# Kernel tuning notes

Hardware: AMD Instinct MI355X
Metric: run time of the kernel (lower is better)

## Reference

```python
import jax, jax.numpy as jnp
import numpy as np

N_ROLES = 6
EPS = 1e-5

def _ln(x, scale, bias):
    m = jnp.mean(x, axis=-1, keepdims=True)
    v = jnp.var(x, axis=-1, keepdims=True)
    return (x - m) * jax.lax.rsqrt(v + EPS) * scale + bias

def setup_inputs() -> dict:
    key = jax.random.key(0)
    ks = jax.random.split(key, 20)
    T, B, D_OBS, H, A = 32, 1024, 256, 512, 32
    inp = {
        'rnn_states': jax.random.normal(ks[0], (B, H), jnp.float32),
        'obs': jax.random.normal(ks[1], (T, B, D_OBS), jnp.float32),
        'resets': jnp.zeros((T, B), jnp.float32),
        'available_actions': jnp.ones((T, B, A), jnp.float32),
        'role_ids': jax.random.randint(ks[2], (T, B), 0, N_ROLES, jnp.int32),
        # feature norm over obs_dim
        'fn_scale': jnp.ones((D_OBS,), jnp.float32),
        'fn_bias': jnp.zeros((D_OBS,), jnp.float32),
        # base MLP: obs_dim->512->512, each followed by LayerNorm
        'W0': jax.random.normal(ks[3], (D_OBS, H), jnp.float32) * 0.02,
        'b0': jnp.zeros((H,), jnp.float32),
        'ln0_scale': jnp.ones((H,), jnp.float32),
        'ln0_bias': jnp.zeros((H,), jnp.float32),
        'W1': jax.random.normal(ks[4], (H, H), jnp.float32) * 0.02,
        'b1': jnp.zeros((H,), jnp.float32),
        'ln1_scale': jnp.ones((H,), jnp.float32),
        'ln1_bias': jnp.zeros((H,), jnp.float32),
        # per-role routes: obs_dim->128->H (stacked over roles)
        'Wr0': jax.random.normal(ks[5], (N_ROLES, D_OBS, 128), jnp.float32) * 0.02,
        'br0': jnp.zeros((N_ROLES, 128), jnp.float32),
        'Wr1': jax.random.normal(ks[6], (N_ROLES, 128, H), jnp.float32) * 0.02,
        'br1': jnp.zeros((N_ROLES, H), jnp.float32),
        # per-role heads: H->64->32->action_dim (stacked over roles)
        'Wh0': jax.random.normal(ks[7], (N_ROLES, H, 64), jnp.float32) * 0.02,
        'bh0': jnp.zeros((N_ROLES, 64), jnp.float32),
        'Wh1': jax.random.normal(ks[8], (N_ROLES, 64, 32), jnp.float32) * 0.02,
        'bh1': jnp.zeros((N_ROLES, 32), jnp.float32),
        'Wh2': jax.random.normal(ks[9], (N_ROLES, 32, A), jnp.float32) * 0.02,
        'bh2': jnp.zeros((N_ROLES, A), jnp.float32),
    }
    return inp

def _gather_by_role(all_values, role_ids):
    # all_values: (K, T, B, F); role_ids: (T, B) -> (T, B, F)
    idx = role_ids[None, :, :, None].astype(jnp.int32)
    return jnp.take_along_axis(all_values, idx, axis=0)[0]

def reference(rnn_states, obs, resets, available_actions, role_ids,
              fn_scale, fn_bias, W0, b0, ln0_scale, ln0_bias,
              W1, b1, ln1_scale, ln1_bias,
              Wr0, br0, Wr1, br1,
              Wh0, bh0, Wh1, bh1, Wh2, bh2):
    # feature normalization on raw obs
    obs_n = _ln(obs, fn_scale, fn_bias)
    # shared base MLP (relu + LayerNorm after each Dense)
    e = _ln(jax.nn.relu(obs_n @ W0 + b0), ln0_scale, ln0_bias)
    e = _ln(jax.nn.relu(e @ W1 + b1), ln1_scale, ln1_bias)
    # per-role pre-GRU residual routes on (normalized) obs
    r = jax.nn.relu(jnp.einsum('tbi,kih->ktbh', obs_n, Wr0) + br0[:, None, None, :])
    r = jax.nn.relu(jnp.einsum('ktbh,kho->ktbo', r, Wr1) + br1[:, None, None, :])
    e = e + _gather_by_role(r, role_ids)
    # no recurrent policy configured: rnn_states pass through
    # per-role heads -> all logits (K, T, B, A)
    h = jax.nn.relu(jnp.einsum('tbh,khf->ktbf', e, Wh0) + bh0[:, None, None, :])
    h = jax.nn.relu(jnp.einsum('ktbf,kfg->ktbg', h, Wh1) + bh1[:, None, None, :])
    all_logits = jnp.einsum('ktbg,kga->ktba', h, Wh2) + bh2[:, None, None, :]
    logits = _gather_by_role(all_logits, role_ids)
    logits = jnp.where(available_actions > 0.5, logits, jnp.full_like(logits, -1e10))
    return rnn_states, logits
```

## Files before the change

kernel.cpp:

```cpp
#include <hip/hip_runtime.h>
#include <stdint.h>

typedef unsigned short u16;
typedef unsigned int u32;

using bf16x8 = __attribute__((ext_vector_type(8))) short;
using f32x4  = __attribute__((ext_vector_type(4))) float;

#define DEVINL __device__ __forceinline__

DEVINL float b2f(u16 u) { return __builtin_bit_cast(float, (u32)u << 16); }
DEVINL u16 f2b(float f) {
  u32 u = __builtin_bit_cast(u32, f);
  u += 0x7FFFu + ((u >> 16) & 1u);
  return (u16)(u >> 16);
}

DEVINL void gll16(const u16* src, u16* dst) {
  __builtin_amdgcn_global_load_lds(
      (const __attribute__((address_space(1))) void*)(uintptr_t)src,
      (__attribute__((address_space(3))) void*)(uintptr_t)dst, 16, 0, 0);
}

#define MFMA __builtin_amdgcn_mfma_f32_16x16x32_bf16
#define NROLE 6
#define PROWS 33152
#define PBLK  518

__global__ __launch_bounds__(256) void role_count(
    const int* __restrict__ rid, int* __restrict__ blkCnt)
{
  __shared__ int h[NROLE];
  if (threadIdx.x < NROLE) h[threadIdx.x] = 0;
  __syncthreads();
  atomicAdd(&h[rid[blockIdx.x * 256 + threadIdx.x]], 1);
  __syncthreads();
  if (threadIdx.x < NROLE) blkCnt[blockIdx.x * NROLE + threadIdx.x] = h[threadIdx.x];
}

__global__ __launch_bounds__(256) void fill2(
    const int* __restrict__ rid, const int* __restrict__ blkCnt,
    int* __restrict__ bucket, int* __restrict__ pbaseOut, int* __restrict__ cntArr)
{
  __shared__ int c[128 * NROLE];
  __shared__ int preArr[NROLE], scnt[NROLE], pb[NROLE + 1], h[NROLE];
  const int tid = threadIdx.x;
  const int bx = blockIdx.x;
  for (int i = tid; i < 128 * NROLE; i += 256) c[i] = blkCnt[i];
  if (tid < NROLE) h[tid] = 0;
  __syncthreads();
  if (tid < NROLE) {
    int k = tid, run = 0, pre = 0;
    for (int b = 0; b < 128; ++b) { if (b == bx) pre = run; run += c[b * NROLE + k]; }
    scnt[k] = run; preArr[k] = pre;
  }
  __syncthreads();
  if (tid == 0) {
    pb[0] = 0;
    for (int k = 0; k < NROLE; ++k) pb[k + 1] = pb[k] + ((scnt[k] + 63) & ~63);
  }
  __syncthreads();
  if (bx == 0) {
    if (tid <= NROLE) pbaseOut[tid] = pb[tid];
    if (tid < NROLE) cntArr[tid] = scnt[tid];
    for (int k = 0; k < NROLE; ++k)
      for (int p = pb[k] + scnt[k] + tid; p < pb[k + 1]; p += 256) bucket[p] = 0;
    for (int p = pb[NROLE] + tid; p < PROWS; p += 256) bucket[p] = 0;
  }
  int i = bx * 256 + tid;
  int k = rid[i];
  int pos = atomicAdd(&h[k], 1);
  bucket[pb[k] + preArr[k] + pos] = i;
}

DEVINL void tp_tile(const float* __restrict__ s, u16* __restrict__ d,
                    int R, int C, int bx, int by, int z)
{
  __shared__ u16 tile[32][33];
  const size_t mstride = (size_t)R * C;
  s += (size_t)z * mstride;
  d += (size_t)z * mstride;
  int r0 = bx * 32, c0 = by * 32;
  int tx = threadIdx.x & 31, ty = threadIdx.x >> 5;
#pragma unroll
  for (int i = 0; i < 32; i += 8)
    tile[ty + i][tx] = f2b(s[(size_t)(r0 + ty + i) * C + (c0 + tx)]);
  __syncthreads();
#pragma unroll
  for (int i = 0; i < 32; i += 8)
    d[(size_t)(c0 + ty + i) * R + (r0 + tx)] = tile[tx][ty + i];
}

__global__ __launch_bounds__(256) void mega0(
    const float* W0, const float* W1, const float* Wr0, const float* Wr1, const float* Wh0,
    u16* W0t, u16* W1t, u16* Wr0t, u16* Wr1t, u16* Wh0t,
    const float* __restrict__ obs, const float* __restrict__ fn_s,
    const float* __restrict__ fn_b, u16* __restrict__ obs_nB,
    const int* __restrict__ bucket,
    const float* __restrict__ rnn, float* __restrict__ outRnn)
{
  int b = blockIdx.x;
  const int tid = threadIdx.x;
  if (b < 1152) {
    if (b < 128)      {            tp_tile(W0, W0t, 256, 512, b % 8,  b / 8, 0); }
    else if (b < 384) { b -= 128;  tp_tile(W1, W1t, 512, 512, b % 16, b / 16, 0); }
    else if (b < 576) { b -= 384;  int t = b / 8;  tp_tile(Wr0, Wr0t, 256, 128, b % 8,  t % 4,  t / 4); }
    else if (b < 960) { b -= 576;  int t = b / 4;  tp_tile(Wr1, Wr1t, 128, 512, b % 4,  t % 16, t / 16); }
    else              { b -= 960;  int t = b / 16; tp_tile(Wh0, Wh0t, 512, 64,  b % 16, t % 2,  t / 2); }
  } else if (b < 1152 + PROWS / 16) {
    b -= 1152;
    const int lane = tid & 63, wave = tid >> 6;
#pragma unroll
    for (int it = 0; it < 4; ++it) {
      int p = b * 16 + wave * 4 + it;
      int g = bucket[p];
      const float* xr = obs + (size_t)g * 256 + lane * 4;
      float x[4] __attribute__((aligned(16)));
      *(float4*)x = *(const float4*)xr;
      float s = 0.f, s2 = 0.f;
#pragma unroll
      for (int q = 0; q < 4; ++q) { s += x[q]; s2 += x[q] * x[q]; }
#pragma unroll
      for (int o = 32; o > 0; o >>= 1) { s += __shfl_xor(s, o, 64); s2 += __shfl_xor(s2, o, 64); }
      float m = s * (1.f / 256.f);
      float v = s2 * (1.f / 256.f) - m * m;
      float inv = rsqrtf(v + 1e-5f);
      u16 yu[4] __attribute__((aligned(8)));
#pragma unroll
      for (int q = 0; q < 4; ++q)
        yu[q] = f2b((x[q] - m) * inv * fn_s[lane * 4 + q] + fn_b[lane * 4 + q]);
      *(uint2*)(obs_nB + (size_t)p * 256 + lane * 4) = *(uint2*)yu;
    }
  } else {
    b -= 1152 + PROWS / 16;
    const float4* src = (const float4*)rnn;
    float4* dst = (float4*)outRnn;
    int base = (b * 256 + tid) * 4;
#pragma unroll
    for (int i = 0; i < 4; ++i) dst[base + i] = src[base + i];
  }
}

template <int K>
DEVINL void gemm_ln_body(
    const u16* __restrict__ A, const u16* __restrict__ Bt,
    const float* __restrict__ bias, const float* __restrict__ lnsc,
    const float* __restrict__ lnbi, u16* __restrict__ C, int bx)
{
  constexpr int BK = 64, NI = K / BK;
  __shared__ __align__(16) u16 As[2][64 * BK];
  __shared__ float redS[64][4];
  __shared__ float redSS[64][4];
  __shared__ float prm[1536];
  const int tid = threadIdx.x;
  const int rowBase = bx * 64;
  const int lane = tid & 63, wave = tid >> 6;
#pragma unroll
  for (int i = tid; i < 512; i += 256) {
    prm[i] = bias[i]; prm[512 + i] = lnsc[i]; prm[1024 + i] = lnbi[i];
  }
  u32 aOff[2];
#pragma unroll
  for (int r = 0; r < 2; ++r) {
    int row = r * 32 + (tid >> 3);
    aOff[r] = (u32)(rowBase + row) * (u32)K + (u32)(((tid & 7) ^ (row & 7)) * 8);
  }
  const int quad = lane >> 4, lm = lane & 15, l7 = lm & 7;
  const int wn = wave * 128;
  u32 bOff[8];
#pragma unroll
  for (int j = 0; j < 8; ++j)
    bOff[j] = (u32)(wn + j * 16 + lm) * (u32)K + (u32)(quad * 8);

  f32x4 acc[4][8] = {};

#pragma unroll
  for (int r = 0; r < 2; ++r)
    gll16(A + aOff[r], &As[0][r * 2048 + wave * 512]);
  bf16x8 bP[8];
#pragma unroll
  for (int j = 0; j < 8; ++j)
    bP[j] = *(const bf16x8*)(Bt + bOff[j]);
  __syncthreads();

  for (int i = 0; i < NI; ++i) {
    const u16* Ab = As[i & 1];
    if (i + 1 < NI) {
#pragma unroll
      for (int r = 0; r < 2; ++r)
        gll16(A + aOff[r] + (i + 1) * BK, &As[(i + 1) & 1][r * 2048 + wave * 512]);
    }
    bf16x8 bN[8];
#pragma unroll
    for (int j = 0; j < 8; ++j)
      bN[j] = *(const bf16x8*)(Bt + bOff[j] + i * BK + 32);
    bf16x8 af[4];
#pragma unroll
    for (int i2 = 0; i2 < 4; ++i2)
      af[i2] = *(const bf16x8*)&Ab[(i2 * 16 + lm) * 64 + ((quad ^ l7) * 8)];
#pragma unroll
    for (int i2 = 0; i2 < 4; ++i2)
#pragma unroll
      for (int j = 0; j < 8; ++j)
        acc[i2][j] = MFMA(af[i2], bP[j], acc[i2][j], 0, 0, 0);
    if (i + 1 < NI) {
#pragma unroll
      for (int j = 0; j < 8; ++j)
        bP[j] = *(const bf16x8*)(Bt + bOff[j] + (i + 1) * BK);
    }
#pragma unroll
    for (int i2 = 0; i2 < 4; ++i2)
      af[i2] = *(const bf16x8*)&Ab[(i2 * 16 + lm) * 64 + (((quad + 4) ^ l7) * 8)];
#pragma unroll
    for (int i2 = 0; i2 < 4; ++i2)
#pragma unroll
      for (int j = 0; j < 8; ++j)
        acc[i2][j] = MFMA(af[i2], bN[j], acc[i2][j], 0, 0, 0);
    __syncthreads();
  }

#pragma unroll
  for (int i2 = 0; i2 < 4; ++i2) {
#pragma unroll
    for (int r2 = 0; r2 < 4; ++r2) {
      float s = 0.f, ss = 0.f;
#pragma unroll
      for (int j = 0; j < 8; ++j) {
        float v = fmaxf(acc[i2][j][r2] + prm[wn + j * 16 + lm], 0.f);
        acc[i2][j][r2] = v;
        s += v; ss += v * v;
      }
#pragma unroll
      for (int o = 1; o < 16; o <<= 1) { s += __shfl_xor(s, o, 64); ss += __shfl_xor(ss, o, 64); }
      if (lm == 0) {
        int rowL = i2 * 16 + quad * 4 + r2;
        redS[rowL][wave] = s;
        redSS[rowL][wave] = ss;
      }
    }
  }
  __syncthreads();
#pragma unroll
  for (int i2 = 0; i2 < 4; ++i2) {
#pragma unroll
    for (int r2 = 0; r2 < 4; ++r2) {
      int rowL = i2 * 16 + quad * 4 + r2;
      float ts  = redS[rowL][0] + redS[rowL][1] + redS[rowL][2] + redS[rowL][3];
      float tss = redSS[rowL][0] + redSS[rowL][1] + redSS[rowL][2] + redSS[rowL][3];
      float m = ts * (1.f / 512.f);
      float var = tss * (1.f / 512.f) - m * m;
      float inv = rsqrtf(var + 1e-5f);
      size_t base = (size_t)(rowBase + rowL) * 512;
#pragma unroll
      for (int j = 0; j < 8; ++j) {
        int col = wn + j * 16 + lm;
        float y = (acc[i2][j][r2] - m) * inv * prm[512 + col] + prm[1024 + col];
        C[base + col] = f2b(y);
      }
    }
  }
}

DEVINL void route0_body(
    const u16* __restrict__ A, const u16* __restrict__ Wr0t,
    const float* __restrict__ br0, u16* __restrict__ r1out,
    const int* __restrict__ pbase, int bx)
{
  constexpr int K = 256, NI = 4;
  __shared__ __align__(16) u16 As0[2][64 * 64];
  const int tid = threadIdx.x;
  const int rowBase = bx * 64;
  if (rowBase >= pbase[NROLE]) return;
  int role = 0;
  while (rowBase >= pbase[role + 1]) ++role;
  const int lane = tid & 63, wave = tid >> 6;
  const int quad = lane >> 4, lm = lane & 15, l7 = lm & 7;
  u32 aOff[2];
#pragma unroll
  for (int r = 0; r < 2; ++r) {
    int row = r * 32 + (tid >> 3);
    aOff[r] = (u32)(rowBase + row) * (u32)K + (u32)(((tid & 7) ^ (row & 7)) * 8);
  }
  const int wn0 = wave * 32;
  const u16* B0 = Wr0t + (size_t)role * 128 * 256;
  u32 bOff[2];
#pragma unroll
  for (int j = 0; j < 2; ++j)
    bOff[j] = (u32)(wn0 + j * 16 + lm) * (u32)K + (u32)(quad * 8);

  f32x4 acc[4][2] = {};
#pragma unroll
  for (int r = 0; r < 2; ++r)
    gll16(A + aOff[r], &As0[0][r * 2048 + wave * 512]);
  bf16x8 bP[2];
#pragma unroll
  for (int j = 0; j < 2; ++j) bP[j] = *(const bf16x8*)(B0 + bOff[j]);
  __syncthreads();

  for (int i = 0; i < NI; ++i) {
    const u16* Ab = As0[i & 1];
    if (i + 1 < NI) {
#pragma unroll
      for (int r = 0; r < 2; ++r)
        gll16(A + aOff[r] + (i + 1) * 64, &As0[(i + 1) & 1][r * 2048 + wave * 512]);
    }
    bf16x8 bN[2];
#pragma unroll
    for (int j = 0; j < 2; ++j) bN[j] = *(const bf16x8*)(B0 + bOff[j] + i * 64 + 32);
    bf16x8 af[4];
#pragma unroll
    for (int i2 = 0; i2 < 4; ++i2)
      af[i2] = *(const bf16x8*)&Ab[(i2 * 16 + lm) * 64 + ((quad ^ l7) * 8)];
#pragma unroll
    for (int i2 = 0; i2 < 4; ++i2)
#pragma unroll
      for (int j = 0; j < 2; ++j)
        acc[i2][j] = MFMA(af[i2], bP[j], acc[i2][j], 0, 0, 0);
    if (i + 1 < NI) {
#pragma unroll
      for (int j = 0; j < 2; ++j) bP[j] = *(const bf16x8*)(B0 + bOff[j] + (i + 1) * 64);
    }
#pragma unroll
    for (int i2 = 0; i2 < 4; ++i2)
      af[i2] = *(const bf16x8*)&Ab[(i2 * 16 + lm) * 64 + (((quad + 4) ^ l7) * 8)];
#pragma unroll
    for (int i2 = 0; i2 < 4; ++i2)
#pragma unroll
      for (int j = 0; j < 2; ++j)
        acc[i2][j] = MFMA(af[i2], bN[j], acc[i2][j], 0, 0, 0);
    __syncthreads();
  }
  float bia[2];
#pragma unroll
  for (int j = 0; j < 2; ++j) bia[j] = br0[role * 128 + wn0 + j * 16 + lm];
#pragma unroll
  for (int i2 = 0; i2 < 4; ++i2) {
#pragma unroll
    for (int r2 = 0; r2 < 4; ++r2) {
      int row = rowBase + i2 * 16 + quad * 4 + r2;
#pragma unroll
      for (int j = 0; j < 2; ++j) {
        int col = wn0 + j * 16 + lm;
        r1out[(size_t)row * 128 + col] = f2b(fmaxf(acc[i2][j][r2] + bia[j], 0.f));
      }
    }
  }
}

__global__ __launch_bounds__(256, 2) void g256_r0(
    const u16* __restrict__ obs_nB, const u16* __restrict__ W0t,
    const float* __restrict__ b0, const float* __restrict__ ln0s,
    const float* __restrict__ ln0b, u16* __restrict__ bufA,
    const u16* __restrict__ Wr0t, const float* __restrict__ br0,
    u16* __restrict__ r1out, const int* __restrict__ pbase)
{
  if (blockIdx.x < PBLK)
    gemm_ln_body<256>(obs_nB, W0t, b0, ln0s, ln0b, bufA, blockIdx.x);
  else
    route0_body(obs_nB, Wr0t, br0, r1out, pbase, blockIdx.x - PBLK);
}

__global__ __launch_bounds__(256, 2) void gemm512(
    const u16* __restrict__ bufA, const u16* __restrict__ W1t,
    const float* __restrict__ b1, const float* __restrict__ ln1s,
    const float* __restrict__ ln1b, u16* __restrict__ bufB)
{
  gemm_ln_body<512>(bufA, W1t, b1, ln1s, ln1b, bufB, blockIdx.x);
}

__global__ __launch_bounds__(256, 2) void route1_k(
    const u16* __restrict__ r1, const u16* __restrict__ Wr1t,
    const float* __restrict__ br1, const u16* __restrict__ e,
    u16* __restrict__ ea, const int* __restrict__ pbase)
{
  constexpr int K = 128, NI = 2;
  __shared__ __align__(16) u16 As[2][64 * 64];
  const int tid = threadIdx.x;
  const int rowBase = blockIdx.x * 64;
  if (rowBase >= pbase[NROLE]) return;
  int role = 0;
  while (rowBase >= pbase[role + 1]) ++role;
  const int lane = tid & 63, wave = tid >> 6;
  const int quad = lane >> 4, lm = lane & 15, l7 = lm & 7;
  u32 aOff[2];
#pragma unroll
  for (int r = 0; r < 2; ++r) {
    int row = r * 32 + (tid >> 3);
    aOff[r] = (u32)(rowBase + row) * (u32)K + (u32)(((tid & 7) ^ (row & 7)) * 8);
  }
  const int wn = wave * 128;
  const u16* B1 = Wr1t + (size_t)role * 512 * 128;
  u32 bOff[8];
#pragma unroll
  for (int j = 0; j < 8; ++j)
    bOff[j] = (u32)(wn + j * 16 + lm) * (u32)K + (u32)(quad * 8);

  f32x4 acc[4][8] = {};
#pragma unroll
  for (int r = 0; r < 2; ++r)
    gll16(r1 + aOff[r], &As[0][r * 2048 + wave * 512]);
  bf16x8 bP[8];
#pragma unroll
  for (int j = 0; j < 8; ++j) bP[j] = *(const bf16x8*)(B1 + bOff[j]);
  __syncthreads();

  for (int i = 0; i < NI; ++i) {
    const u16* Ab = As[i & 1];
    if (i + 1 < NI) {
#pragma unroll
      for (int r = 0; r < 2; ++r)
        gll16(r1 + aOff[r] + (i + 1) * 64, &As[(i + 1) & 1][r * 2048 + wave * 512]);
    }
    bf16x8 bN[8];
#pragma unroll
    for (int j = 0; j < 8; ++j) bN[j] = *(const bf16x8*)(B1 + bOff[j] + i * 64 + 32);
    bf16x8 af[4];
#pragma unroll
    for (int i2 = 0; i2 < 4; ++i2)
      af[i2] = *(const bf16x8*)&Ab[(i2 * 16 + lm) * 64 + ((quad ^ l7) * 8)];
#pragma unroll
    for (int i2 = 0; i2 < 4; ++i2)
#pragma unroll
      for (int j = 0; j < 8; ++j)
        acc[i2][j] = MFMA(af[i2], bP[j], acc[i2][j], 0, 0, 0);
    if (i + 1 < NI) {
#pragma unroll
      for (int j = 0; j < 8; ++j) bP[j] = *(const bf16x8*)(B1 + bOff[j] + (i + 1) * 64);
    }
#pragma unroll
    for (int i2 = 0; i2 < 4; ++i2)
      af[i2] = *(const bf16x8*)&Ab[(i2 * 16 + lm) * 64 + (((quad + 4) ^ l7) * 8)];
#pragma unroll
    for (int i2 = 0; i2 < 4; ++i2)
#pragma unroll
      for (int j = 0; j < 8; ++j)
        acc[i2][j] = MFMA(af[i2], bN[j], acc[i2][j], 0, 0, 0);
    __syncthreads();
  }
  float bia[8];
#pragma unroll
  for (int j = 0; j < 8; ++j) bia[j] = br1[role * 512 + wn + j * 16 + lm];
#pragma unroll
  for (int i2 = 0; i2 < 4; ++i2) {
#pragma unroll
    for (int r2 = 0; r2 < 4; ++r2) {
      size_t row = (size_t)(rowBase + i2 * 16 + quad * 4 + r2);
#pragma unroll
      for (int j = 0; j < 8; ++j) {
        int col = wn + j * 16 + lm;
        float v = fmaxf(acc[i2][j][r2] + bia[j], 0.f) + b2f(e[row * 512 + col]);
        ea[row * 512 + col] = f2b(v);
      }
    }
  }
}

__global__ __launch_bounds__(256, 2) void head_all(
    const u16* __restrict__ ea, const u16* __restrict__ Wh0t,
    const float* __restrict__ bh0,
    const float* __restrict__ Wh1, const float* __restrict__ bh1,
    const float* __restrict__ Wh2, const float* __restrict__ bh2,
    const float* __restrict__ avail, const int* __restrict__ bucket,
    const int* __restrict__ pbase, const int* __restrict__ cntArr,
    float* __restrict__ outLogits)
{
  constexpr int K = 512, NI = 8;
  __shared__ __align__(16) u16 As[2][64 * 64];
  __shared__ u16 h0s[64 * 68];
  __shared__ float h1s[64 * 36];
  const int tid = threadIdx.x;
  const int rowBase = blockIdx.x * 64;
  if (rowBase >= pbase[NROLE]) return;
  int role = 0;
  while (rowBase >= pbase[role + 1]) ++role;
  const int lane = tid & 63, wave = tid >> 6;
  const int quad = lane >> 4, lm = lane & 15, l7 = lm & 7;
  u32 aOff[2];
#pragma unroll
  for (int r = 0; r < 2; ++r) {
    int row = r * 32 + (tid >> 3);
    aOff[r] = (u32)(rowBase + row) * (u32)K + (u32)(((tid & 7) ^ (row & 7)) * 8);
  }
  const int col0 = wave * 16 + lm;
  const u16* B2 = Wh0t + (size_t)role * 64 * 512;
  const u32 bOff = (u32)col0 * (u32)K + (u32)(quad * 8);

  f32x4 acc[4] = {};
#pragma unroll
  for (int r = 0; r < 2; ++r)
    gll16(ea + aOff[r], &As[0][r * 2048 + wave * 512]);
  bf16x8 bP = *(const bf16x8*)(B2 + bOff);
  __syncthreads();

  for (int i = 0; i < NI; ++i) {
    const u16* Ab = As[i & 1];
    if (i + 1 < NI) {
#pragma unroll
      for (int r = 0; r < 2; ++r)
        gll16(ea + aOff[r] + (i + 1) * 64, &As[(i + 1) & 1][r * 2048 + wave * 512]);
    }
    bf16x8 bN = *(const bf16x8*)(B2 + bOff + i * 64 + 32);
    bf16x8 af[4];
#pragma unroll
    for (int i2 = 0; i2 < 4; ++i2)
      af[i2] = *(const bf16x8*)&Ab[(i2 * 16 + lm) * 64 + ((quad ^ l7) * 8)];
#pragma unroll
    for (int i2 = 0; i2 < 4; ++i2)
      acc[i2] = MFMA(af[i2], bP, acc[i2], 0, 0, 0);
    if (i + 1 < NI) bP = *(const bf16x8*)(B2 + bOff + (i + 1) * 64);
#pragma unroll
    for (int i2 = 0; i2 < 4; ++i2)
      af[i2] = *(const bf16x8*)&Ab[(i2 * 16 + lm) * 64 + (((quad + 4) ^ l7) * 8)];
#pragma unroll
    for (int i2 = 0; i2 < 4; ++i2)
      acc[i2] = MFMA(af[i2], bN, acc[i2], 0, 0, 0);
    __syncthreads();
  }
  {
    float b2v = bh0[role * 64 + col0];
#pragma unroll
    for (int i2 = 0; i2 < 4; ++i2)
#pragma unroll
      for (int r2 = 0; r2 < 4; ++r2) {
        int row = i2 * 16 + quad * 4 + r2;
        h0s[row * 68 + col0] = f2b(fmaxf(acc[i2][r2] + b2v, 0.f));
      }
  }
  __syncthreads();

  {
    const int r = tid >> 2;
    const int n0 = (tid & 3) * 8;
    const float* W1k = Wh1 + (size_t)role * 64 * 32;
    const float* W2k = Wh2 + (size_t)role * 32 * 32;
    float4 a1a = *(const float4*)(bh1 + role * 32 + n0);
    float4 a1b = *(const float4*)(bh1 + role * 32 + n0 + 4);
#pragma unroll 8
    for (int j = 0; j < 64; ++j) {
      float hj = b2f(h0s[r * 68 + j]);
      float4 wa = *(const float4*)(W1k + j * 32 + n0);
      float4 wb = *(const float4*)(W1k + j * 32 + n0 + 4);
      a1a.x += hj * wa.x; a1a.y += hj * wa.y; a1a.z += hj * wa.z; a1a.w += hj * wa.w;
      a1b.x += hj * wb.x; a1b.y += hj * wb.y; a1b.z += hj * wb.z; a1b.w += hj * wb.w;
    }
    h1s[r * 36 + n0 + 0] = fmaxf(a1a.x, 0.f);
    h1s[r * 36 + n0 + 1] = fmaxf(a1a.y, 0.f);
    h1s[r * 36 + n0 + 2] = fmaxf(a1a.z, 0.f);
    h1s[r * 36 + n0 + 3] = fmaxf(a1a.w, 0.f);
    h1s[r * 36 + n0 + 4] = fmaxf(a1b.x, 0.f);
    h1s[r * 36 + n0 + 5] = fmaxf(a1b.y, 0.f);
    h1s[r * 36 + n0 + 6] = fmaxf(a1b.z, 0.f);
    h1s[r * 36 + n0 + 7] = fmaxf(a1b.w, 0.f);
    __syncthreads();
    float4 a2a = *(const float4*)(bh2 + role * 32 + n0);
    float4 a2b = *(const float4*)(bh2 + role * 32 + n0 + 4);
#pragma unroll 8
    for (int n = 0; n < 32; ++n) {
      float hn = h1s[r * 36 + n];
      float4 wa = *(const float4*)(W2k + n * 32 + n0);
      float4 wb = *(const float4*)(W2k + n * 32 + n0 + 4);
      a2a.x += hn * wa.x; a2a.y += hn * wa.y; a2a.z += hn * wa.z; a2a.w += hn * wa.w;
      a2b.x += hn * wb.x; a2b.y += hn * wb.y; a2b.z += hn * wb.z; a2b.w += hn * wb.w;
    }
    int local = rowBase + r - pbase[role];
    if (local < cntArr[role]) {
      int g = bucket[rowBase + r];
      float4 ava = *(const float4*)(avail + (size_t)g * 32 + n0);
      float4 avb = *(const float4*)(avail + (size_t)g * 32 + n0 + 4);
      float4 oa, ob;
      oa.x = (ava.x > 0.5f) ? a2a.x : -1e10f;
      oa.y = (ava.y > 0.5f) ? a2a.y : -1e10f;
      oa.z = (ava.z > 0.5f) ? a2a.z : -1e10f;
      oa.w = (ava.w > 0.5f) ? a2a.w : -1e10f;
      ob.x = (avb.x > 0.5f) ? a2b.x : -1e10f;
      ob.y = (avb.y > 0.5f) ? a2b.y : -1e10f;
      ob.z = (avb.z > 0.5f) ? a2b.z : -1e10f;
      ob.w = (avb.w > 0.5f) ? a2b.w : -1e10f;
      *(float4*)(outLogits + (size_t)g * 32 + n0) = oa;
      *(float4*)(outLogits + (size_t)g * 32 + n0 + 4) = ob;
    }
  }
}

extern "C" void kernel_launch(void* const* d_in, const int* in_sizes, int n_in,
                              void* d_out, int out_size, void* d_ws, size_t ws_size,
                              hipStream_t stream)
{
  const float* rnn  = (const float*)d_in[0];
  const float* obs  = (const float*)d_in[1];
  const float* avail= (const float*)d_in[3];
  const int*   rid  = (const int*)d_in[4];
  const float* fn_s = (const float*)d_in[5];
  const float* fn_b = (const float*)d_in[6];
  const float* W0   = (const float*)d_in[7];
  const float* b0   = (const float*)d_in[8];
  const float* ln0s = (const float*)d_in[9];
  const float* ln0b = (const float*)d_in[10];
  const float* W1   = (const float*)d_in[11];
  const float* b1   = (const float*)d_in[12];
  const float* ln1s = (const float*)d_in[13];
  const float* ln1b = (const float*)d_in[14];
  const float* Wr0  = (const float*)d_in[15];
  const float* br0  = (const float*)d_in[16];
  const float* Wr1  = (const float*)d_in[17];
  const float* br1  = (const float*)d_in[18];
  const float* Wh0  = (const float*)d_in[19];
  const float* bh0  = (const float*)d_in[20];
  const float* Wh1  = (const float*)d_in[21];
  const float* bh1  = (const float*)d_in[22];
  const float* Wh2  = (const float*)d_in[23];
  const float* bh2  = (const float*)d_in[24];

  char* w = (char*)d_ws;
  auto carve = [&](size_t bytes) { char* p = w; w += (bytes + 255) & ~(size_t)255; return p; };
  u16* obs_nB = (u16*)carve((size_t)PROWS * 256 * 2);
  u16* bufA   = (u16*)carve((size_t)PROWS * 512 * 2);
  u16* bufB   = (u16*)carve((size_t)PROWS * 512 * 2);
  u16* r1buf  = (u16*)carve((size_t)PROWS * 128 * 2);
  u16* W0t    = (u16*)carve((size_t)512 * 256 * 2);
  u16* W1t    = (u16*)carve((size_t)512 * 512 * 2);
  u16* Wr0t   = (u16*)carve((size_t)6 * 128 * 256 * 2);
  u16* Wr1t   = (u16*)carve((size_t)6 * 512 * 128 * 2);
  u16* Wh0t   = (u16*)carve((size_t)6 * 64 * 512 * 2);
  int* bucket = (int*)carve((size_t)PROWS * 4);
  int* blkCnt = (int*)carve((size_t)128 * NROLE * 4);
  int* pbase  = (int*)carve(256);
  int* cntArr = (int*)carve(256);

  float* outLogits = (float*)d_out + (size_t)1024 * 512;

  role_count<<<128, 256, 0, stream>>>(rid, blkCnt);
  fill2<<<128, 256, 0, stream>>>(rid, blkCnt, bucket, pbase, cntArr);

  mega0<<<1152 + PROWS / 16 + 128, 256, 0, stream>>>(
      W0, W1, Wr0, Wr1, Wh0, W0t, W1t, Wr0t, Wr1t, Wh0t,
      obs, fn_s, fn_b, obs_nB, bucket, rnn, (float*)d_out);

  g256_r0<<<2 * PBLK, 256, 0, stream>>>(obs_nB, W0t, b0, ln0s, ln0b, bufA,
                                        Wr0t, br0, r1buf, pbase);

  gemm512<<<PBLK, 256, 0, stream>>>(bufA, W1t, b1, ln1s, ln1b, bufB);

  route1_k<<<PBLK, 256, 0, stream>>>(r1buf, Wr1t, br1, bufB, bufA, pbase);

  head_all<<<PBLK, 256, 0, stream>>>(bufA, Wh0t, bh0, Wh1, bh1, Wh2, bh2,
                                     avail, bucket, pbase, cntArr, outLogits);
}
```

Measured before the change: 301.3 us.

## Fuse pipeline into two row-block kernels keeping activations in LDS

Result: slower. 368.6 us (+22.4%).

```diff
diff --git a/kernel.cpp b/kernel.cpp
--- a/kernel.cpp
+++ b/kernel.cpp
@@ -38,14 +38,14 @@
   if (threadIdx.x < NROLE) blkCnt[blockIdx.x * NROLE + threadIdx.x] = h[threadIdx.x];
 }
 
-__global__ __launch_bounds__(256) void fill2(
+DEVINL void fill_body(
     const int* __restrict__ rid, const int* __restrict__ blkCnt,
-    int* __restrict__ bucket, int* __restrict__ pbaseOut, int* __restrict__ cntArr)
+    int* __restrict__ bucket, int* __restrict__ pbaseOut, int* __restrict__ cntArr,
+    int bx)
 {
   __shared__ int c[128 * NROLE];
   __shared__ int preArr[NROLE], scnt[NROLE], pb[NROLE + 1], h[NROLE];
   const int tid = threadIdx.x;
-  const int bx = blockIdx.x;
   for (int i = tid; i < 128 * NROLE; i += 256) c[i] = blkCnt[i];
   if (tid < NROLE) h[tid] = 0;
   __syncthreads();
@@ -91,13 +91,12 @@
     d[(size_t)(c0 + ty + i) * R + (r0 + tx)] = tile[tx][ty + i];
 }
 
-__global__ __launch_bounds__(256) void mega0(
+__global__ __launch_bounds__(256) void prep(
     const float* W0, const float* W1, const float* Wr0, const float* Wr1, const float* Wh0,
     u16* W0t, u16* W1t, u16* Wr0t, u16* Wr1t, u16* Wh0t,
-    const float* __restrict__ obs, const float* __restrict__ fn_s,
-    const float* __restrict__ fn_b, u16* __restrict__ obs_nB,
-    const int* __restrict__ bucket,
-    const float* __restrict__ rnn, float* __restrict__ outRnn)
+    const float* __restrict__ rnn, float* __restrict__ outRnn,
+    const int* __restrict__ rid, const int* __restrict__ blkCnt,
+    int* __restrict__ bucket, int* __restrict__ pbase, int* __restrict__ cntArr)
 {
   int b = blockIdx.x;
   const int tid = threadIdx.x;
@@ -107,274 +106,30 @@
     else if (b < 576) { b -= 384;  int t = b / 8;  tp_tile(Wr0, Wr0t, 256, 128, b % 8,  t % 4,  t / 4); }
     else if (b < 960) { b -= 576;  int t = b / 4;  tp_tile(Wr1, Wr1t, 128, 512, b % 4,  t % 16, t / 16); }
     else              { b -= 960;  int t = b / 16; tp_tile(Wh0, Wh0t, 512, 64,  b % 16, t % 2,  t / 2); }
-  } else if (b < 1152 + PROWS / 16) {
+  } else if (b < 1280) {
     b -= 1152;
-    const int lane = tid & 63, wave = tid >> 6;
-#pragma unroll
-    for (int it = 0; it < 4; ++it) {
-      int p = b * 16 + wave * 4 + it;
-      int g = bucket[p];
-      const float* xr = obs + (size_t)g * 256 + lane * 4;
-      float x[4] __attribute__((aligned(16)));
-      *(float4*)x = *(const float4*)xr;
-      float s = 0.f, s2 = 0.f;
-#pragma unroll
-      for (int q = 0; q < 4; ++q) { s += x[q]; s2 += x[q] * x[q]; }
-#pragma unroll
-      for (int o = 32; o > 0; o >>= 1) { s += __shfl_xor(s, o, 64); s2 += __shfl_xor(s2, o, 64); }
-      float m = s * (1.f / 256.f);
-      float v = s2 * (1.f / 256.f) - m * m;
-      float inv = rsqrtf(v + 1e-5f);
-      u16 yu[4] __attribute__((aligned(8)));
-#pragma unroll
-      for (int q = 0; q < 4; ++q)
-        yu[q] = f2b((x[q] - m) * inv * fn_s[lane * 4 + q] + fn_b[lane * 4 + q]);
-      *(uint2*)(obs_nB + (size_t)p * 256 + lane * 4) = *(uint2*)yu;
-    }
-  } else {
-    b -= 1152 + PROWS / 16;
     const float4* src = (const float4*)rnn;
     float4* dst = (float4*)outRnn;
     int base = (b * 256 + tid) * 4;
 #pragma unroll
     for (int i = 0; i < 4; ++i) dst[base + i] = src[base + i];
-  }
-}
-
-template <int K>
-DEVINL void gemm_ln_body(
-    const u16* __restrict__ A, const u16* __restrict__ Bt,
-    const float* __restrict__ bias, const float* __restrict__ lnsc,
-    const float* __restrict__ lnbi, u16* __restrict__ C, int bx)
-{
-  constexpr int BK = 64, NI = K / BK;
-  __shared__ __align__(16) u16 As[2][64 * BK];
-  __shared__ float redS[64][4];
-  __shared__ float redSS[64][4];
-  __shared__ float prm[1536];
-  const int tid = threadIdx.x;
-  const int rowBase = bx * 64;
-  const int lane = tid & 63, wave = tid >> 6;
-#pragma unroll
-  for (int i = tid; i < 512; i += 256) {
-    prm[i] = bias[i]; prm[512 + i] = lnsc[i]; prm[1024 + i] = lnbi[i];
-  }
-  u32 aOff[2];
-#pragma unroll
-  for (int r = 0; r < 2; ++r) {
-    int row = r * 32 + (tid >> 3);
-    aOff[r] = (u32)(rowBase + row) * (u32)K + (u32)(((tid & 7) ^ (row & 7)) * 8);
-  }
-  const int quad = lane >> 4, lm = lane & 15, l7 = lm & 7;
-  const int wn = wave * 128;
-  u32 bOff[8];
-#pragma unroll
-  for (int j = 0; j < 8; ++j)
-    bOff[j] = (u32)(wn + j * 16 + lm) * (u32)K + (u32)(quad * 8);
-
-  f32x4 acc[4][8] = {};
-
-#pragma unroll
-  for (int r = 0; r < 2; ++r)
-    gll16(A + aOff[r], &As[0][r * 2048 + wave * 512]);
-  bf16x8 bP[8];
-#pragma unroll
-  for (int j = 0; j < 8; ++j)
-    bP[j] = *(const bf16x8*)(Bt + bOff[j]);
-  __syncthreads();
-
-  for (int i = 0; i < NI; ++i) {
-    const u16* Ab = As[i & 1];
-    if (i + 1 < NI) {
-#pragma unroll
-      for (int r = 0; r < 2; ++r)
-        gll16(A + aOff[r] + (i + 1) * BK, &As[(i + 1) & 1][r * 2048 + wave * 512]);
-    }
-    bf16x8 bN[8];
-#pragma unroll
-    for (int j = 0; j < 8; ++j)
-      bN[j] = *(const bf16x8*)(Bt + bOff[j] + i * BK + 32);
-    bf16x8 af[4];
-#pragma unroll
-    for (int i2 = 0; i2 < 4; ++i2)
-      af[i2] = *(const bf16x8*)&Ab[(i2 * 16 + lm) * 64 + ((quad ^ l7) * 8)];
-#pragma unroll
-    for (int i2 = 0; i2 < 4; ++i2)
-#pragma unroll
-      for (int j = 0; j < 8; ++j)
-        acc[i2][j] = MFMA(af[i2], bP[j], acc[i2][j], 0, 0, 0);
-    if (i + 1 < NI) {
-#pragma unroll
-      for (int j = 0; j < 8; ++j)
-        bP[j] = *(const bf16x8*)(Bt + bOff[j] + (i + 1) * BK);
-    }
-#pragma unroll
-    for (int i2 = 0; i2 < 4; ++i2)
-      af[i2] = *(const bf16x8*)&Ab[(i2 * 16 + lm) * 64 + (((quad + 4) ^ l7) * 8)];
-#pragma unroll
-    for (int i2 = 0; i2 < 4; ++i2)
-#pragma unroll
-      for (int j = 0; j < 8; ++j)
-        acc[i2][j] = MFMA(af[i2], bN[j], acc[i2][j], 0, 0, 0);
-    __syncthreads();
-  }
-
-#pragma unroll
-  for (int i2 = 0; i2 < 4; ++i2) {
-#pragma unroll
-    for (int r2 = 0; r2 < 4; ++r2) {
-      float s = 0.f, ss = 0.f;
-#pragma unroll
-      for (int j = 0; j < 8; ++j) {
-        float v = fmaxf(acc[i2][j][r2] + prm[wn + j * 16 + lm], 0.f);
-        acc[i2][j][r2] = v;
-        s += v; ss += v * v;
-      }
-#pragma unroll
-      for (int o = 1; o < 16; o <<= 1) { s += __shfl_xor(s, o, 64); ss += __shfl_xor(ss, o, 64); }
-      if (lm == 0) {
-        int rowL = i2 * 16 + quad * 4 + r2;
-        redS[rowL][wave] = s;
-        redSS[rowL][wave] = ss;
-      }
-    }
-  }
-  __syncthreads();
-#pragma unroll
-  for (int i2 = 0; i2 < 4; ++i2) {
-#pragma unroll
-    for (int r2 = 0; r2 < 4; ++r2) {
-      int rowL = i2 * 16 + quad * 4 + r2;
-      float ts  = redS[rowL][0] + redS[rowL][1] + redS[rowL][2] + redS[rowL][3];
-      float tss = redSS[rowL][0] + redSS[rowL][1] + redSS[rowL][2] + redSS[rowL][3];
-      float m = ts * (1.f / 512.f);
-      float var = tss * (1.f / 512.f) - m * m;
-      float inv = rsqrtf(var + 1e-5f);
-      size_t base = (size_t)(rowBase + rowL) * 512;
-#pragma unroll
-      for (int j = 0; j < 8; ++j) {
-        int col = wn + j * 16 + lm;
-        float y = (acc[i2][j][r2] - m) * inv * prm[512 + col] + prm[1024 + col];
-        C[base + col] = f2b(y);
-      }
-    }
-  }
-}
-
-DEVINL void route0_body(
-    const u16* __restrict__ A, const u16* __restrict__ Wr0t,
-    const float* __restrict__ br0, u16* __restrict__ r1out,
-    const int* __restrict__ pbase, int bx)
-{
-  constexpr int K = 256, NI = 4;
-  __shared__ __align__(16) u16 As0[2][64 * 64];
-  const int tid = threadIdx.x;
-  const int rowBase = bx * 64;
-  if (rowBase >= pbase[NROLE]) return;
-  int role = 0;
-  while (rowBase >= pbase[role + 1]) ++role;
-  const int lane = tid & 63, wave = tid >> 6;
-  const int quad = lane >> 4, lm = lane & 15, l7 = lm & 7;
-  u32 aOff[2];
-#pragma unroll
-  for (int r = 0; r < 2; ++r) {
-    int row = r * 32 + (tid >> 3);
-    aOff[r] = (u32)(rowBase + row) * (u32)K + (u32)(((tid & 7) ^ (row & 7)) * 8);
-  }
-  const int wn0 = wave * 32;
-  const u16* B0 = Wr0t + (size_t)role * 128 * 256;
-  u32 bOff[2];
-#pragma unroll
-  for (int j = 0; j < 2; ++j)
-    bOff[j] = (u32)(wn0 + j * 16 + lm) * (u32)K + (u32)(quad * 8);
-
-  f32x4 acc[4][2] = {};
-#pragma unroll
-  for (int r = 0; r < 2; ++r)
-    gll16(A + aOff[r], &As0[0][r * 2048 + wave * 512]);
-  bf16x8 bP[2];
-#pragma unroll
-  for (int j = 0; j < 2; ++j) bP[j] = *(const bf16x8*)(B0 + bOff[j]);
-  __syncthreads();
-
-  for (int i = 0; i < NI; ++i) {
-    const u16* Ab = As0[i & 1];
-    if (i + 1 < NI) {
-#pragma unroll
-      for (int r = 0; r < 2; ++r)
-        gll16(A + aOff[r] + (i + 1) * 64, &As0[(i + 1) & 1][r * 2048 + wave * 512]);
-    }
-    bf16x8 bN[2];
-#pragma unroll
-    for (int j = 0; j < 2; ++j) bN[j] = *(const bf16x8*)(B0 + bOff[j] + i * 64 + 32);
-    bf16x8 af[4];
-#pragma unroll
-    for (int i2 = 0; i2 < 4; ++i2)
-      af[i2] = *(const bf16x8*)&Ab[(i2 * 16 + lm) * 64 + ((quad ^ l7) * 8)];
-#pragma unroll
-    for (int i2 = 0; i2 < 4; ++i2)
-#pragma unroll
-      for (int j = 0; j < 2; ++j)
-        acc[i2][j] = MFMA(af[i2], bP[j], acc[i2][j], 0, 0, 0);
-    if (i + 1 < NI) {
-#pragma unroll
-      for (int j = 0; j < 2; ++j) bP[j] = *(const bf16x8*)(B0 + bOff[j] + (i + 1) * 64);
-    }
-#pragma unroll
-    for (int i2 = 0; i2 < 4; ++i2)
-      af[i2] = *(const bf16x8*)&Ab[(i2 * 16 + lm) * 64 + (((quad + 4) ^ l7) * 8)];
-#pragma unroll
-    for (int i2 = 0; i2 < 4; ++i2)
-#pragma unroll
-      for (int j = 0; j < 2; ++j)
-        acc[i2][j] = MFMA(af[i2], bN[j], acc[i2][j], 0, 0, 0);
-    __syncthreads();
-  }
-  float bia[2];
-#pragma unroll
-  for (int j = 0; j < 2; ++j) bia[j] = br0[role * 128 + wn0 + j * 16 + lm];
-#pragma unroll
-  for (int i2 = 0; i2 < 4; ++i2) {
-#pragma unroll
-    for (int r2 = 0; r2 < 4; ++r2) {
-      int row = rowBase + i2 * 16 + quad * 4 + r2;
-#pragma unroll
-      for (int j = 0; j < 2; ++j) {
-        int col = wn0 + j * 16 + lm;
-        r1out[(size_t)row * 128 + col] = f2b(fmaxf(acc[i2][j][r2] + bia[j], 0.f));
-      }
-    }
-  }
-}
-
-__global__ __launch_bounds__(256, 2) void g256_r0(
-    const u16* __restrict__ obs_nB, const u16* __restrict__ W0t,
-    const float* __restrict__ b0, const float* __restrict__ ln0s,
-    const float* __restrict__ ln0b, u16* __restrict__ bufA,
+  } else {
+    fill_body(rid, blkCnt, bucket, pbase, cntArr, b - 1280);
+  }
+}
+
+__global__ __launch_bounds__(256, 2) void stage1_k(
+    const float* __restrict__ obs, const float* __restrict__ fn_s,
+    const float* __restrict__ fn_b,
+    const u16* __restrict__ W0t, const float* __restrict__ b0,
+    const float* __restrict__ ln0s, const float* __restrict__ ln0b,
     const u16* __restrict__ Wr0t, const float* __restrict__ br0,
-    u16* __restrict__ r1out, const int* __restrict__ pbase)
-{
-  if (blockIdx.x < PBLK)
-    gemm_ln_body<256>(obs_nB, W0t, b0, ln0s, ln0b, bufA, blockIdx.x);
-  else
-    route0_body(obs_nB, Wr0t, br0, r1out, pbase, blockIdx.x - PBLK);
-}
-
-__global__ __launch_bounds__(256, 2) void gemm512(
-    const u16* __restrict__ bufA, const u16* __restrict__ W1t,
-    const float* __restrict__ b1, const float* __restrict__ ln1s,
-    const float* __restrict__ ln1b, u16* __restrict__ bufB)
-{
-  gemm_ln_body<512>(bufA, W1t, b1, ln1s, ln1b, bufB, blockIdx.x);
-}
-
-__global__ __launch_bounds__(256, 2) void route1_k(
-    const u16* __restrict__ r1, const u16* __restrict__ Wr1t,
-    const float* __restrict__ br1, const u16* __restrict__ e,
-    u16* __restrict__ ea, const int* __restrict__ pbase)
-{
-  constexpr int K = 128, NI = 2;
-  __shared__ __align__(16) u16 As[2][64 * 64];
+    const int* __restrict__ bucket, const int* __restrict__ pbase,
+    u16* __restrict__ bufA, u16* __restrict__ r1out)
+{
+  __shared__ __align__(16) u16 As[64 * 256];
+  __shared__ float redS[64][4], redSS[64][4];
+  __shared__ float prm[1664];
   const int tid = threadIdx.x;
   const int rowBase = blockIdx.x * 64;
   if (rowBase >= pbase[NROLE]) return;
@@ -382,92 +137,138 @@
   while (rowBase >= pbase[role + 1]) ++role;
   const int lane = tid & 63, wave = tid >> 6;
   const int quad = lane >> 4, lm = lane & 15, l7 = lm & 7;
-  u32 aOff[2];
-#pragma unroll
-  for (int r = 0; r < 2; ++r) {
-    int row = r * 32 + (tid >> 3);
-    aOff[r] = (u32)(rowBase + row) * (u32)K + (u32)(((tid & 7) ^ (row & 7)) * 8);
-  }
-  const int wn = wave * 128;
-  const u16* B1 = Wr1t + (size_t)role * 512 * 128;
-  u32 bOff[8];
-#pragma unroll
-  for (int j = 0; j < 8; ++j)
-    bOff[j] = (u32)(wn + j * 16 + lm) * (u32)K + (u32)(quad * 8);
-
-  f32x4 acc[4][8] = {};
-#pragma unroll
-  for (int r = 0; r < 2; ++r)
-    gll16(r1 + aOff[r], &As[0][r * 2048 + wave * 512]);
-  bf16x8 bP[8];
-#pragma unroll
-  for (int j = 0; j < 8; ++j) bP[j] = *(const bf16x8*)(B1 + bOff[j]);
-  __syncthreads();
-
-  for (int i = 0; i < NI; ++i) {
-    const u16* Ab = As[i & 1];
-    if (i + 1 < NI) {
-#pragma unroll
-      for (int r = 0; r < 2; ++r)
-        gll16(r1 + aOff[r] + (i + 1) * 64, &As[(i + 1) & 1][r * 2048 + wave * 512]);
-    }
-    bf16x8 bN[8];
-#pragma unroll
-    for (int j = 0; j < 8; ++j) bN[j] = *(const bf16x8*)(B1 + bOff[j] + i * 64 + 32);
-    bf16x8 af[4];
-#pragma unroll
-    for (int i2 = 0; i2 < 4; ++i2)
-      af[i2] = *(const bf16x8*)&Ab[(i2 * 16 + lm) * 64 + ((quad ^ l7) * 8)];
-#pragma unroll
-    for (int i2 = 0; i2 < 4; ++i2)
+
+#pragma unroll
+  for (int i = tid; i < 512; i += 256) {
+    prm[i] = b0[i]; prm[512 + i] = ln0s[i]; prm[1024 + i] = ln0b[i];
+  }
+  if (tid < 128) prm[1536 + tid] = br0[role * 128 + tid];
+
+  for (int it = 0; it < 16; ++it) {
+    int row = wave * 16 + it;
+    int g = bucket[rowBase + row];
+    float x[4] __attribute__((aligned(16)));
+    *(float4*)x = *(const float4*)(obs + (size_t)g * 256 + lane * 4);
+    float s = 0.f, s2 = 0.f;
+#pragma unroll
+    for (int q = 0; q < 4; ++q) { s += x[q]; s2 += x[q] * x[q]; }
+#pragma unroll
+    for (int o = 32; o > 0; o >>= 1) { s += __shfl_xor(s, o, 64); s2 += __shfl_xor(s2, o, 64); }
+    float m = s * (1.f / 256.f);
+    float v = s2 * (1.f / 256.f) - m * m;
+    float inv = rsqrtf(v + 1e-5f);
+    u16 yu[4] __attribute__((aligned(8)));
+#pragma unroll
+    for (int q = 0; q < 4; ++q)
+      yu[q] = f2b((x[q] - m) * inv * fn_s[lane * 4 + q] + fn_b[lane * 4 + q]);
+    *(uint2*)&As[row * 256 + (((lane >> 1) ^ (row & 7)) * 8) + (lane & 1) * 4] = *(uint2*)yu;
+  }
+  __syncthreads();
+
+  {
+    const int wn0 = wave * 32;
+    const u16* B0 = Wr0t + (size_t)role * 128 * 256;
+    f32x4 acc[4][2] = {};
+#pragma unroll
+    for (int kc = 0; kc < 8; ++kc) {
+      bf16x8 af[4], bw[2];
+#pragma unroll
+      for (int j = 0; j < 2; ++j)
+        bw[j] = *(const bf16x8*)(B0 + (u32)(wn0 + j * 16 + lm) * 256u + (u32)(kc * 32 + quad * 8));
+#pragma unroll
+      for (int i2 = 0; i2 < 4; ++i2)
+        af[i2] = *(const bf16x8*)&As[(i2 * 16 + lm) * 256 + ((((quad + kc * 4) ^ l7) & 31) * 8)];
+#pragma unroll
+      for (int i2 = 0; i2 < 4; ++i2)
+#pragma unroll
+        for (int j = 0; j < 2; ++j)
+          acc[i2][j] = MFMA(af[i2], bw[j], acc[i2][j], 0, 0, 0);
+    }
+#pragma unroll
+    for (int i2 = 0; i2 < 4; ++i2)
+#pragma unroll
+      for (int r2 = 0; r2 < 4; ++r2) {
+        size_t row = (size_t)(rowBase + i2 * 16 + quad * 4 + r2);
+#pragma unroll
+        for (int j = 0; j < 2; ++j) {
+          int col = wn0 + j * 16 + lm;
+          r1out[row * 128 + col] = f2b(fmaxf(acc[i2][j][r2] + prm[1536 + col], 0.f));
+        }
+      }
+  }
+
+  {
+    const int wn = wave * 128;
+    f32x4 acc[4][8] = {};
+#pragma unroll
+    for (int kc = 0; kc < 8; ++kc) {
+      bf16x8 af[4], bw[8];
 #pragma unroll
       for (int j = 0; j < 8; ++j)
-        acc[i2][j] = MFMA(af[i2], bP[j], acc[i2][j], 0, 0, 0);
-    if (i + 1 < NI) {
-#pragma unroll
-      for (int j = 0; j < 8; ++j) bP[j] = *(const bf16x8*)(B1 + bOff[j] + (i + 1) * 64);
-    }
-#pragma unroll
-    for (int i2 = 0; i2 < 4; ++i2)
-      af[i2] = *(const bf16x8*)&Ab[(i2 * 16 + lm) * 64 + (((quad + 4) ^ l7) * 8)];
-#pragma unroll
-    for (int i2 = 0; i2 < 4; ++i2)
-#pragma unroll
-      for (int j = 0; j < 8; ++j)
-        acc[i2][j] = MFMA(af[i2], bN[j], acc[i2][j], 0, 0, 0);
+        bw[j] = *(const bf16x8*)(W0t + (u32)(wn + j * 16 + lm) * 256u + (u32)(kc * 32 + quad * 8));
+#pragma unroll
+      for (int i2 = 0; i2 < 4; ++i2)
+        af[i2] = *(const bf16x8*)&As[(i2 * 16 + lm) * 256 + ((((quad + kc * 4) ^ l7) & 31) * 8)];
+#pragma unroll
+      for (int i2 = 0; i2 < 4; ++i2)
+#pragma unroll
+        for (int j = 0; j < 8; ++j)
+          acc[i2][j] = MFMA(af[i2], bw[j], acc[i2][j], 0, 0, 0);
+    }
+#pragma unroll
+    for (int i2 = 0; i2 < 4; ++i2)
+#pragma unroll
+      for (int r2 = 0; r2 < 4; ++r2) {
+        float s = 0.f, ss = 0.f;
+#pragma unroll
+        for (int j = 0; j < 8; ++j) {
+          float v = fmaxf(acc[i2][j][r2] + prm[wn + j * 16 + lm], 0.f);
+          acc[i2][j][r2] = v; s += v; ss += v * v;
+        }
+#pragma unroll
+        for (int o = 1; o < 16; o <<= 1) { s += __shfl_xor(s, o, 64); ss += __shfl_xor(ss, o, 64); }
+        if (lm == 0) {
+          int rowL = i2 * 16 + quad * 4 + r2;
+          redS[rowL][wave] = s; redSS[rowL][wave] = ss;
+        }
+      }
     __syncthreads();
-  }
-  float bia[8];
-#pragma unroll
-  for (int j = 0; j < 8; ++j) bia[j] = br1[role * 512 + wn + j * 16 + lm];
-#pragma unroll
-  for (int i2 = 0; i2 < 4; ++i2) {
-#pragma unroll
-    for (int r2 = 0; r2 < 4; ++r2) {
-      size_t row = (size_t)(rowBase + i2 * 16 + quad * 4 + r2);
-#pragma unroll
-      for (int j = 0; j < 8; ++j) {
-        int col = wn + j * 16 + lm;
-        float v = fmaxf(acc[i2][j][r2] + bia[j], 0.f) + b2f(e[row * 512 + col]);
-        ea[row * 512 + col] = f2b(v);
-      }
-    }
-  }
-}
-
-__global__ __launch_bounds__(256, 2) void head_all(
-    const u16* __restrict__ ea, const u16* __restrict__ Wh0t,
-    const float* __restrict__ bh0,
+#pragma unroll
+    for (int i2 = 0; i2 < 4; ++i2)
+#pragma unroll
+      for (int r2 = 0; r2 < 4; ++r2) {
+        int rowL = i2 * 16 + quad * 4 + r2;
+        float ts  = redS[rowL][0] + redS[rowL][1] + redS[rowL][2] + redS[rowL][3];
+        float tss = redSS[rowL][0] + redSS[rowL][1] + redSS[rowL][2] + redSS[rowL][3];
+        float m = ts * (1.f / 512.f);
+        float var = tss * (1.f / 512.f) - m * m;
+        float inv = rsqrtf(var + 1e-5f);
+        size_t base = (size_t)(rowBase + rowL) * 512;
+#pragma unroll
+        for (int j = 0; j < 8; ++j) {
+          int col = wn + j * 16 + lm;
+          bufA[base + col] = f2b((acc[i2][j][r2] - m) * inv * prm[512 + col] + prm[1024 + col]);
+        }
+      }
+  }
+}
+
+__global__ __launch_bounds__(256, 2) void stage2_k(
+    const u16* __restrict__ bufA, const u16* __restrict__ W1t,
+    const float* __restrict__ b1, const float* __restrict__ ln1s,
+    const float* __restrict__ ln1b,
+    const u16* __restrict__ r1, const u16* __restrict__ Wr1t,
+    const float* __restrict__ br1,
+    const u16* __restrict__ Wh0t, const float* __restrict__ bh0,
     const float* __restrict__ Wh1, const float* __restrict__ bh1,
     const float* __restrict__ Wh2, const float* __restrict__ bh2,
     const float* __restrict__ avail, const int* __restrict__ bucket,
     const int* __restrict__ pbase, const int* __restrict__ cntArr,
     float* __restrict__ outLogits)
 {
-  constexpr int K = 512, NI = 8;
-  __shared__ __align__(16) u16 As[2][64 * 64];
-  __shared__ u16 h0s[64 * 68];
-  __shared__ float h1s[64 * 36];
+  __shared__ __align__(16) u16 As[64 * 512];
+  __shared__ float redS[64][4], redSS[64][4];
+  __shared__ float prm[2112];
   const int tid = threadIdx.x;
   const int rowBase = blockIdx.x * 64;
   if (rowBase >= pbase[NROLE]) return;
@@ -475,60 +276,146 @@
   while (rowBase >= pbase[role + 1]) ++role;
   const int lane = tid & 63, wave = tid >> 6;
   const int quad = lane >> 4, lm = lane & 15, l7 = lm & 7;
-  u32 aOff[2];
-#pragma unroll
-  for (int r = 0; r < 2; ++r) {
-    int row = r * 32 + (tid >> 3);
-    aOff[r] = (u32)(rowBase + row) * (u32)K + (u32)(((tid & 7) ^ (row & 7)) * 8);
-  }
-  const int col0 = wave * 16 + lm;
-  const u16* B2 = Wh0t + (size_t)role * 64 * 512;
-  const u32 bOff = (u32)col0 * (u32)K + (u32)(quad * 8);
-
-  f32x4 acc[4] = {};
-#pragma unroll
-  for (int r = 0; r < 2; ++r)
-    gll16(ea + aOff[r], &As[0][r * 2048 + wave * 512]);
-  bf16x8 bP = *(const bf16x8*)(B2 + bOff);
-  __syncthreads();
-
-  for (int i = 0; i < NI; ++i) {
-    const u16* Ab = As[i & 1];
-    if (i + 1 < NI) {
-#pragma unroll
-      for (int r = 0; r < 2; ++r)
-        gll16(ea + aOff[r] + (i + 1) * 64, &As[(i + 1) & 1][r * 2048 + wave * 512]);
-    }
-    bf16x8 bN = *(const bf16x8*)(B2 + bOff + i * 64 + 32);
-    bf16x8 af[4];
-#pragma unroll
-    for (int i2 = 0; i2 < 4; ++i2)
-      af[i2] = *(const bf16x8*)&Ab[(i2 * 16 + lm) * 64 + ((quad ^ l7) * 8)];
-#pragma unroll
-    for (int i2 = 0; i2 < 4; ++i2)
-      acc[i2] = MFMA(af[i2], bP, acc[i2], 0, 0, 0);
-    if (i + 1 < NI) bP = *(const bf16x8*)(B2 + bOff + (i + 1) * 64);
-#pragma unroll
-    for (int i2 = 0; i2 < 4; ++i2)
-      af[i2] = *(const bf16x8*)&Ab[(i2 * 16 + lm) * 64 + (((quad + 4) ^ l7) * 8)];
-#pragma unroll
-    for (int i2 = 0; i2 < 4; ++i2)
-      acc[i2] = MFMA(af[i2], bN, acc[i2], 0, 0, 0);
+
+#pragma unroll
+  for (int rr = 0; rr < 16; ++rr) {
+    int row = rr * 4 + wave;
+    gll16(bufA + (size_t)(rowBase + row) * 512 + (u32)(((lane ^ (row & 7)) & 63) * 8),
+          &As[row * 512 + lane * 8]);
+  }
+#pragma unroll
+  for (int i = tid; i < 512; i += 256) {
+    prm[i] = b1[i]; prm[512 + i] = ln1s[i]; prm[1024 + i] = ln1b[i];
+    prm[1536 + i] = br1[role * 512 + i];
+  }
+  if (tid < 64) prm[2048 + tid] = bh0[role * 64 + tid];
+  __syncthreads();
+
+  const int wn = wave * 128;
+
+  {
+    f32x4 acc[4][8] = {};
+#pragma unroll
+    for (int kc = 0; kc < 16; ++kc) {
+      bf16x8 af[4], bw[8];
+#pragma unroll
+      for (int j = 0; j < 8; ++j)
+        bw[j] = *(const bf16x8*)(W1t + (u32)(wn + j * 16 + lm) * 512u + (u32)(kc * 32 + quad * 8));
+#pragma unroll
+      for (int i2 = 0; i2 < 4; ++i2)
+        af[i2] = *(const bf16x8*)&As[(i2 * 16 + lm) * 512 + ((((quad + kc * 4) ^ l7) & 63) * 8)];
+#pragma unroll
+      for (int i2 = 0; i2 < 4; ++i2)
+#pragma unroll
+        for (int j = 0; j < 8; ++j)
+          acc[i2][j] = MFMA(af[i2], bw[j], acc[i2][j], 0, 0, 0);
+    }
+#pragma unroll
+    for (int i2 = 0; i2 < 4; ++i2)
+#pragma unroll
+      for (int r2 = 0; r2 < 4; ++r2) {
+        float s = 0.f, ss = 0.f;
+#pragma unroll
+        for (int j = 0; j < 8; ++j) {
+          float v = fmaxf(acc[i2][j][r2] + prm[wn + j * 16 + lm], 0.f);
+          acc[i2][j][r2] = v; s += v; ss += v * v;
+        }
+#pragma unroll
+        for (int o = 1; o < 16; o <<= 1) { s += __shfl_xor(s, o, 64); ss += __shfl_xor(ss, o, 64); }
+        if (lm == 0) {
+          int rowL = i2 * 16 + quad * 4 + r2;
+          redS[rowL][wave] = s; redSS[rowL][wave] = ss;
+        }
+      }
     __syncthreads();
-  }
-  {
-    float b2v = bh0[role * 64 + col0];
 #pragma unroll
     for (int i2 = 0; i2 < 4; ++i2)
 #pragma unroll
       for (int r2 = 0; r2 < 4; ++r2) {
         int row = i2 * 16 + quad * 4 + r2;
-        h0s[row * 68 + col0] = f2b(fmaxf(acc[i2][r2] + b2v, 0.f));
-      }
-  }
-  __syncthreads();
-
-  {
+        float ts  = redS[row][0] + redS[row][1] + redS[row][2] + redS[row][3];
+        float tss = redSS[row][0] + redSS[row][1] + redSS[row][2] + redSS[row][3];
+        float m = ts * (1.f / 512.f);
+        float var = tss * (1.f / 512.f) - m * m;
+        float inv = rsqrtf(var + 1e-5f);
+#pragma unroll
+        for (int j = 0; j < 8; ++j) {
+          int col = wn + j * 16 + lm;
+          float e = (acc[i2][j][r2] - m) * inv * prm[512 + col] + prm[1024 + col];
+          As[row * 512 + ((((col >> 3) ^ (row & 7)) ) * 8) + (col & 7)] = f2b(e);
+        }
+      }
+  }
+  __syncthreads();
+
+  {
+    const u16* B1 = Wr1t + (size_t)role * 512 * 128;
+    f32x4 acc[4][8] = {};
+#pragma unroll
+    for (int kc = 0; kc < 4; ++kc) {
+      bf16x8 af[4], bw[8];
+#pragma unroll
+      for (int j = 0; j < 8; ++j)
+        bw[j] = *(const bf16x8*)(B1 + (u32)(wn + j * 16 + lm) * 128u + (u32)(kc * 32 + quad * 8));
+#pragma unroll
+      for (int i2 = 0; i2 < 4; ++i2)
+        af[i2] = *(const bf16x8*)(r1 + (size_t)(rowBase + i2 * 16 + lm) * 128 + (u32)(kc * 32 + quad * 8));
+#pragma unroll
+      for (int i2 = 0; i2 < 4; ++i2)
+#pragma unroll
+        for (int j = 0; j < 8; ++j)
+          acc[i2][j] = MFMA(af[i2], bw[j], acc[i2][j], 0, 0, 0);
+    }
+#pragma unroll
+    for (int i2 = 0; i2 < 4; ++i2)
+#pragma unroll
+      for (int r2 = 0; r2 < 4; ++r2) {
+        int row = i2 * 16 + quad * 4 + r2;
+#pragma unroll
+        for (int j = 0; j < 8; ++j) {
+          int col = wn + j * 16 + lm;
+          int addr = row * 512 + (((col >> 3) ^ (row & 7)) * 8) + (col & 7);
+          float v = fmaxf(acc[i2][j][r2] + prm[1536 + col], 0.f) + b2f(As[addr]);
+          As[addr] = f2b(v);
+        }
+      }
+  }
+  __syncthreads();
+
+  f32x4 acc3[4] = {};
+  {
+    const int col0 = wave * 16 + lm;
+    const u16* B2 = Wh0t + (size_t)role * 64 * 512;
+#pragma unroll
+    for (int kc = 0; kc < 16; ++kc) {
+      bf16x8 af[4];
+      bf16x8 bw = *(const bf16x8*)(B2 + (u32)col0 * 512u + (u32)(kc * 32 + quad * 8));
+#pragma unroll
+      for (int i2 = 0; i2 < 4; ++i2)
+        af[i2] = *(const bf16x8*)&As[(i2 * 16 + lm) * 512 + ((((quad + kc * 4) ^ l7) & 63) * 8)];
+#pragma unroll
+      for (int i2 = 0; i2 < 4; ++i2)
+        acc3[i2] = MFMA(af[i2], bw, acc3[i2], 0, 0, 0);
+    }
+  }
+  __syncthreads();
+
+  u16* h0s = As;
+  {
+    const int col0 = wave * 16 + lm;
+    float bv = prm[2048 + col0];
+#pragma unroll
+    for (int i2 = 0; i2 < 4; ++i2)
+#pragma unroll
+      for (int r2 = 0; r2 < 4; ++r2) {
+        int row = i2 * 16 + quad * 4 + r2;
+        h0s[row * 68 + col0] = f2b(fmaxf(acc3[i2][r2] + bv, 0.f));
+      }
+  }
+  __syncthreads();
+
+  {
+    float* h1s = (float*)&As[16384];
     const int r = tid >> 2;
     const int n0 = (tid & 3) * 8;
     const float* W1k = Wh1 + (size_t)role * 64 * 32;
@@ -613,9 +500,7 @@
 
   char* w = (char*)d_ws;
   auto carve = [&](size_t bytes) { char* p = w; w += (bytes + 255) & ~(size_t)255; return p; };
-  u16* obs_nB = (u16*)carve((size_t)PROWS * 256 * 2);
   u16* bufA   = (u16*)carve((size_t)PROWS * 512 * 2);
-  u16* bufB   = (u16*)carve((size_t)PROWS * 512 * 2);
   u16* r1buf  = (u16*)carve((size_t)PROWS * 128 * 2);
   u16* W0t    = (u16*)carve((size_t)512 * 256 * 2);
   u16* W1t    = (u16*)carve((size_t)512 * 512 * 2);
@@ -630,19 +515,15 @@
   float* outLogits = (float*)d_out + (size_t)1024 * 512;
 
   role_count<<<128, 256, 0, stream>>>(rid, blkCnt);
-  fill2<<<128, 256, 0, stream>>>(rid, blkCnt, bucket, pbase, cntArr);
-
-  mega0<<<1152 + PROWS / 16 + 128, 256, 0, stream>>>(
-      W0, W1, Wr0, Wr1, Wh0, W0t, W1t, Wr0t, Wr1t, Wh0t,
-      obs, fn_s, fn_b, obs_nB, bucket, rnn, (float*)d_out);
-
-  g256_r0<<<2 * PBLK, 256, 0, stream>>>(obs_nB, W0t, b0, ln0s, ln0b, bufA,
-                                        Wr0t, br0, r1buf, pbase);
-
-  gemm512<<<PBLK, 256, 0, stream>>>(bufA, W1t, b1, ln1s, ln1b, bufB);
-
-  route1_k<<<PBLK, 256, 0, stream>>>(r1buf, Wr1t, br1, bufB, bufA, pbase);
-
-  head_all<<<PBLK, 256, 0, stream>>>(bufA, Wh0t, bh0, Wh1, bh1, Wh2, bh2,
-                                     avail, bucket, pbase, cntArr, outLogits);
-}
+
+  prep<<<1408, 256, 0, stream>>>(W0, W1, Wr0, Wr1, Wh0, W0t, W1t, Wr0t, Wr1t, Wh0t,
+                                 rnn, (float*)d_out, rid, blkCnt, bucket, pbase, cntArr);
+
+  stage1_k<<<PBLK, 256, 0, stream>>>(obs, fn_s, fn_b, W0t, b0, ln0s, ln0b,
+                                     Wr0t, br0, bucket, pbase, bufA, r1buf);
+
+  stage2_k<<<PBLK, 256, 0, stream>>>(bufA, W1t, b1, ln1s, ln1b,
+                                     r1buf, Wr1t, br1, Wh0t, bh0,
+                                     Wh1, bh1, Wh2, bh2, avail,
+                                     bucket, pbase, cntArr, outLogits);
+}
```
